# Kernel optimization log

Hardware: AMD Instinct MI355X
Metric: run time of the kernel (lower is better)

## Reference

```python
import jax, jax.numpy as jnp
import numpy as np

N_NODES = 4096
N_EDGES = 32768
IN_FEAT = 256
OUT_FEAT = 128
HID = 64
IN_HEAD = 64
OUT_HEAD = 5
NEG_SLOPE = 0.2
EPS = 1e-16


def setup_inputs() -> dict:
    key = jax.random.key(0)
    ks = jax.random.split(key, 12)
    x = jax.random.normal(ks[0], (N_NODES, IN_FEAT), dtype=jnp.float32)
    src = jax.random.randint(ks[1], (N_EDGES,), 0, N_NODES)
    dst = jax.random.randint(ks[2], (N_EDGES,), 0, N_NODES)
    edge_index = jnp.stack([src, dst]).astype(jnp.int64)
    s1 = 1.0 / np.sqrt(IN_FEAT)
    s2 = 1.0 / np.sqrt(HID * IN_HEAD)
    W1 = jax.random.normal(ks[3], (IN_FEAT, IN_HEAD * HID), dtype=jnp.float32) * s1
    att_src1 = jax.random.normal(ks[4], (IN_HEAD, HID), dtype=jnp.float32) * 0.1
    att_dst1 = jax.random.normal(ks[5], (IN_HEAD, HID), dtype=jnp.float32) * 0.1
    b1 = jnp.zeros((IN_HEAD * HID,), dtype=jnp.float32)
    W2 = jax.random.normal(ks[6], (IN_HEAD * HID, OUT_HEAD * OUT_FEAT), dtype=jnp.float32) * s2
    att_src2 = jax.random.normal(ks[7], (OUT_HEAD, OUT_FEAT), dtype=jnp.float32) * 0.1
    att_dst2 = jax.random.normal(ks[8], (OUT_HEAD, OUT_FEAT), dtype=jnp.float32) * 0.1
    b2 = jnp.zeros((OUT_FEAT,), dtype=jnp.float32)
    return {"x": x, "edge_index": edge_index, "W1": W1, "att_src1": att_src1,
            "att_dst1": att_dst1, "b1": b1, "W2": W2, "att_src2": att_src2,
            "att_dst2": att_dst2, "b2": b2}


def _gat_conv(x, W, att_src, att_dst, bias, src, dst, heads, out_c, concat):
    # x: [N, F_in]; returns [N, heads*out_c] (concat) or [N, out_c] (mean)
    n = x.shape[0]
    h = (x @ W).reshape(n, heads, out_c)                       # [N,H,C]
    a_src = jnp.sum(h * att_src, axis=-1)                      # [N,H]
    a_dst = jnp.sum(h * att_dst, axis=-1)                      # [N,H]
    e = jax.nn.leaky_relu(a_src[src] + a_dst[dst], NEG_SLOPE)  # [E,H]
    # segment softmax over edges grouped by destination node (PyG softmax)
    m = jax.ops.segment_max(e, dst, num_segments=n)            # [N,H]
    ex = jnp.exp(e - m[dst])
    denom = jax.ops.segment_sum(ex, dst, num_segments=n)       # [N,H]
    alpha = ex / (denom[dst] + EPS)                            # [E,H]
    out = jax.ops.segment_sum(alpha[:, :, None] * h[src], dst, num_segments=n)  # [N,H,C]
    out = out.reshape(n, heads * out_c) if concat else out.mean(axis=1)
    return out + bias


def reference(x, edge_index, W1, att_src1, att_dst1, b1, W2, att_src2, att_dst2, b2):
    n = x.shape[0]
    # PyG GATConv default: add self loops
    loop = jnp.arange(n, dtype=edge_index.dtype)
    src = jnp.concatenate([edge_index[0], loop])
    dst = jnp.concatenate([edge_index[1], loop])
    # dropout layers are identity in eval mode
    h = _gat_conv(x, W1, att_src1, att_dst1, b1, src, dst, IN_HEAD, HID, True)
    h = jax.nn.elu(h)
    h = _gat_conv(h, W2, att_src2, att_dst2, b2, src, dst, OUT_HEAD, OUT_FEAT, False)
    s = jnp.mean(h, axis=0)
    return jnp.tanh(s)
```

## Files before the change

### kernel.cpp

```cpp
#include <hip/hip_runtime.h>
#include <hip/hip_bf16.h>

#define N_NODES 4096
#define NE      32768
#define E_TOT   (NE + N_NODES)
#define IN_FEAT 256
#define HID     64
#define IN_HEAD 64
#define F1      4096
#define OUT_HEAD 5
#define OUT_FEAT 128
#define F2      640
#define NEG_SLOPE 0.2f
#define EPS_A   1e-16f

typedef __bf16 bf16;
typedef bf16 bf16x8 __attribute__((ext_vector_type(8)));
typedef bf16 bf16x4 __attribute__((ext_vector_type(4)));
typedef float f32x4 __attribute__((ext_vector_type(4)));

__device__ inline void async_cp16(bf16* lds, const bf16* g) {
    __builtin_amdgcn_global_load_lds(
        (const __attribute__((address_space(1))) unsigned int*)g,
        (__attribute__((address_space(3))) unsigned int*)lds, 16, 0, 0);
}

__global__ void hist_kernel(const int* __restrict__ edst, int* counts) {
    int e = blockIdx.x * 256 + threadIdx.x;
    if (e >= E_TOT) return;
    int d = (e < NE) ? edst[e] : (e - NE);
    atomicAdd(&counts[d], 1);
}

__global__ void scan_kernel(const int* __restrict__ counts,
                            int* __restrict__ row_start, int* __restrict__ cursor) {
    __shared__ int part[256];
    __shared__ int pre[257];
    int t = threadIdx.x;
    int base = t * 16;
    int local[16];
    int s = 0;
#pragma unroll
    for (int i = 0; i < 16; ++i) { local[i] = s; s += counts[base + i]; }
    part[t] = s;
    __syncthreads();
    if (t == 0) {
        int r = 0;
        for (int i = 0; i < 256; ++i) { pre[i] = r; r += part[i]; }
        pre[256] = r;
    }
    __syncthreads();
    int off = pre[t];
#pragma unroll
    for (int i = 0; i < 16; ++i) {
        int v = off + local[i];
        row_start[base + i] = v;
        cursor[base + i] = v;
    }
    if (t == 0) row_start[N_NODES] = pre[256];
}

__global__ void scatter_kernel(const int* __restrict__ esrc,
                               const int* __restrict__ edst,
                               int* cursor, int* __restrict__ srclist) {
    int e = blockIdx.x * 256 + threadIdx.x;
    if (e >= E_TOT) return;
    int d = (e < NE) ? edst[e] : (e - NE);
    int s = (e < NE) ? esrc[e] : (e - NE);
    int slot = atomicAdd(&cursor[d], 1);
    srclist[slot] = s;
}

#define PB_X   512
#define PB_W1  1024
#define PB_W2  2560
__global__ __launch_bounds__(256)
void prep_kernel(const float* __restrict__ x, bf16* __restrict__ xb,
                 const float* __restrict__ W1, bf16* __restrict__ W1T,
                 const float* __restrict__ W2, bf16* __restrict__ W2T,
                 const float* __restrict__ as1, const float* __restrict__ ad1,
                 bf16* __restrict__ w1s, bf16* __restrict__ w1d) {
    __shared__ float tile[32][33];
    int b = blockIdx.x, t = threadIdx.x;
    if (b < PB_X) {
        int i = b * 256 + t;
        f32x4 a = *(const f32x4*)(x + (size_t)i * 8);
        f32x4 c = *(const f32x4*)(x + (size_t)i * 8 + 4);
        bf16x8 r;
        r[0] = (bf16)a[0]; r[1] = (bf16)a[1]; r[2] = (bf16)a[2]; r[3] = (bf16)a[3];
        r[4] = (bf16)c[0]; r[5] = (bf16)c[1]; r[6] = (bf16)c[2]; r[7] = (bf16)c[3];
        *(bf16x8*)(xb + (size_t)i * 8) = r;
    } else if (b < PB_X + PB_W1 + PB_W2) {
        const float* S; bf16* D; int R, C, gx, gy;
        if (b < PB_X + PB_W1) {
            int bb = b - PB_X;
            S = W1; D = W1T; R = IN_FEAT; C = F1;
            gx = bb % (F1 / 32); gy = bb / (F1 / 32);
        } else {
            int bb = b - PB_X - PB_W1;
            S = W2; D = W2T; R = F1; C = F2;
            gx = bb % (F2 / 32); gy = bb / (F2 / 32);
        }
        int tx = t & 31, ty = t >> 5;
        int c0 = gx * 32, r0 = gy * 32;
#pragma unroll
        for (int i = 0; i < 4; ++i)
            tile[ty + i * 8][tx] = S[(size_t)(r0 + ty + i * 8) * C + c0 + tx];
        __syncthreads();
#pragma unroll
        for (int i = 0; i < 4; ++i)
            D[(size_t)(c0 + ty + i * 8) * R + r0 + tx] = (bf16)tile[tx][ty + i * 8];
    } else {
        int id = (b - PB_X - PB_W1 - PB_W2) * 256 + t;
        int k = id >> 6, h = id & 63;
        const float* wrow = W1 + (size_t)k * F1 + h * HID;
        const float* a1 = as1 + h * HID;
        const float* a2 = ad1 + h * HID;
        float s = 0.f, d = 0.f;
#pragma unroll 8
        for (int c = 0; c < HID; ++c) {
            float w = wrow[c];
            s += w * a1[c];
            d += w * a2[c];
        }
        w1s[id] = (bf16)s;
        w1d[id] = (bf16)d;
    }
}

template <int SPLITK, bool SWZ, typename TC>
__global__ __launch_bounds__(256)
void gemm128_kernel(const bf16* __restrict__ A, const bf16* __restrict__ BT,
                    TC* __restrict__ C, int M, int N, int K) {
    __shared__ bf16 As[128][64];
    __shared__ bf16 Bs[128][64];
    const int tid  = threadIdx.x;
    const int wave = tid >> 6, lane = tid & 63;
    const int quad = lane >> 4, lr = lane & 15;
    int nb, mb, zb;
    if constexpr (SWZ) {
        int bid = blockIdx.x;
        int xx = bid & 7, q = bid >> 3;
        int gp = q / 5; nb = q - gp * 5;
        int g = gp * 8 + xx;
        mb = g >> 2; zb = g & 3;
    } else {
        nb = blockIdx.x; mb = blockIdx.y; zb = blockIdx.z;
    }
    const int m0 = mb * 128, n0 = nb * 128;
    const int kchunk = K / SPLITK;
    const int kbeg = zb * kchunk;
    const int wm = (wave >> 1) * 64;
    const int wn = (wave & 1) * 64;
    TC* Cz = C + (size_t)zb * M * N;

    const int srow = lane >> 3;
    const int scol = ((lane & 7) ^ srow) * 8;
    const int xk = lr & 7;

    f32x4 acc[4][4] = {};

    for (int kk = 0; kk < kchunk; kk += 64) {
        int k0 = kbeg + kk;
#pragma unroll
        for (int c = 0; c < 4; ++c) {
            int r = wave * 32 + c * 8;
            async_cp16(&As[r][0], A + (size_t)(m0 + r + srow) * K + k0 + scol);
            async_cp16(&Bs[r][0], BT + (size_t)(n0 + r + srow) * K + k0 + scol);
        }
        __syncthreads();

#pragma unroll
        for (int ks = 0; ks < 2; ++ks) {
            int ch = ((ks * 4 + quad) ^ xk) * 8;
            bf16x8 af[4], bfr[4];
#pragma unroll
            for (int mt = 0; mt < 4; ++mt)
                af[mt] = *(const bf16x8*)(&As[wm + mt * 16 + lr][ch]);
#pragma unroll
            for (int nt = 0; nt < 4; ++nt)
                bfr[nt] = *(const bf16x8*)(&Bs[wn + nt * 16 + lr][ch]);
#pragma unroll
            for (int mt = 0; mt < 4; ++mt)
#pragma unroll
                for (int nt = 0; nt < 4; ++nt)
                    acc[mt][nt] = __builtin_amdgcn_mfma_f32_16x16x32_bf16(
                        af[mt], bfr[nt], acc[mt][nt], 0, 0, 0);
        }
        __syncthreads();
    }

#pragma unroll
    for (int mt = 0; mt < 4; ++mt)
#pragma unroll
        for (int nt = 0; nt < 4; ++nt) {
            int row0 = m0 + wm + mt * 16 + quad * 4;
            int col = n0 + wn + nt * 16 + lr;
#pragma unroll
            for (int r = 0; r < 4; ++r)
                Cz[(size_t)(row0 + r) * N + col] = (TC)acc[mt][nt][r];
        }
}

__global__ __launch_bounds__(256)
void gemv1_kernel(const float* __restrict__ x,
                  const bf16* __restrict__ w1s, const bf16* __restrict__ w1d,
                  float* __restrict__ a_src, float* __restrict__ a_dst) {
    int wave = threadIdx.x >> 6, lane = threadIdx.x & 63;
    int n = blockIdx.x * 4 + wave;
    const float* xr = x + (size_t)n * IN_FEAT;
    float s = 0.f, d = 0.f;
    for (int k0 = 0; k0 < IN_FEAT; k0 += 4) {
        f32x4 xv = *(const f32x4*)(xr + k0);
#pragma unroll
        for (int j = 0; j < 4; ++j) {
            float xs = xv[j];
            s += xs * (float)w1s[(k0 + j) * IN_HEAD + lane];
            d += xs * (float)w1d[(k0 + j) * IN_HEAD + lane];
        }
    }
    a_src[n * IN_HEAD + lane] = s;
    a_dst[n * IN_HEAD + lane] = d;
}

__global__ __launch_bounds__(64)
void agg1_kernel(const int* __restrict__ row_start,
                 const int* __restrict__ srclist,
                 const float* __restrict__ a_src, const float* __restrict__ a_dst,
                 const bf16* __restrict__ H1, const float* __restrict__ b1,
                 bf16* __restrict__ h_elu) {
    int bid = blockIdx.x;
    int c = bid & 7;
    int d = bid >> 3;
    int lane = threadIdx.x;
    int gh = c * 8 + (lane >> 3);
    int beg = row_start[d], deg = row_start[d + 1] - beg;
    float adst = a_dst[d * IN_HEAD + gh];
    int fbase = c * 512 + lane * 8;
    const float* asg = a_src + gh;

    auto SL = [&](int i) { return srclist[beg + (i < deg ? i : deg - 1)]; };

    int s0 = SL(0), s1 = SL(1), s2 = SL(2), s3 = SL(3);
    float la0 = asg[(size_t)s0 * IN_HEAD];
    bf16x8 v0 = *(const bf16x8*)(H1 + (size_t)s0 * F1 + fbase);
    float la1 = asg[(size_t)s1 * IN_HEAD];
    bf16x8 v1 = *(const bf16x8*)(H1 + (size_t)s1 * F1 + fbase);
    float la2 = asg[(size_t)s2 * IN_HEAD];
    bf16x8 v2 = *(const bf16x8*)(H1 + (size_t)s2 * F1 + fbase);
    float la3 = asg[(size_t)s3 * IN_HEAD];
    bf16x8 v3 = *(const bf16x8*)(H1 + (size_t)s3 * F1 + fbase);
    int s4 = SL(4), s5 = SL(5);

    float m = -1e30f, den = 0.f;
    float acc[8] = {};
    for (int i = 0; i < deg; ++i) {
        int sn = SL(i + 6);
        float la4 = asg[(size_t)s4 * IN_HEAD];
        bf16x8 v4 = *(const bf16x8*)(H1 + (size_t)s4 * F1 + fbase);

        float l = la0 + adst;
        l = l > 0.f ? l : NEG_SLOPE * l;
        if (l > m + 12.f) {
            float r = __expf(m - l);
            den *= r;
#pragma unroll
            for (int k = 0; k < 8; ++k) acc[k] *= r;
            m = l;
        }
        float w = __expf(l - m);
        den += w;
#pragma unroll
        for (int k = 0; k < 8; ++k) acc[k] += w * (float)v0[k];

        la0 = la1; v0 = v1;
        la1 = la2; v1 = v2;
        la2 = la3; v2 = v3;
        la3 = la4; v3 = v4;
        s4 = s5; s5 = sn;
    }
    float dinv = 1.f / (den + EPS_A);

    bf16x8 o;
#pragma unroll
    for (int j = 0; j < 8; ++j) {
        float v = acc[j] * dinv + b1[fbase + j];
        o[j] = (bf16)(v > 0.f ? v : (__expf(v) - 1.f));
    }
    *(bf16x8*)(h_elu + (size_t)d * F1 + fbase) = o;
}

__global__ __launch_bounds__(192)
void fold2_kernel(const bf16* __restrict__ Hp,
                  const float* __restrict__ as2, const float* __restrict__ ad2,
                  float* __restrict__ H2,
                  float* __restrict__ a_src, float* __restrict__ a_dst) {
    int n = blockIdx.x, t = threadIdx.x;
    if (t >= 160) return;
    int h = t >> 5;
    f32x4 sum = {};
#pragma unroll
    for (int z = 0; z < 4; ++z) {
        bf16x4 v = *(const bf16x4*)(Hp + (size_t)z * N_NODES * F2 + (size_t)n * F2 + t * 4);
        sum[0] += (float)v[0]; sum[1] += (float)v[1];
        sum[2] += (float)v[2]; sum[3] += (float)v[3];
    }
    *(f32x4*)(H2 + (size_t)n * F2 + t * 4) = sum;
    f32x4 ws = *(const f32x4*)(as2 + t * 4);
    f32x4 wd = *(const f32x4*)(ad2 + t * 4);
    float s = sum[0] * ws[0] + sum[1] * ws[1] + sum[2] * ws[2] + sum[3] * ws[3];
    float d = sum[0] * wd[0] + sum[1] * wd[1] + sum[2] * wd[2] + sum[3] * wd[3];
#pragma unroll
    for (int o = 1; o <= 16; o <<= 1) {
        s += __shfl_xor(s, o);
        d += __shfl_xor(d, o);
    }
    if ((t & 31) == 0) {
        a_src[n * OUT_HEAD + h] = s;
        a_dst[n * OUT_HEAD + h] = d;
    }
}

__global__ void stats2_kernel(const int* __restrict__ row_start,
                              const int* __restrict__ srclist,
                              const float* __restrict__ a_src,
                              const float* __restrict__ a_dst,
                              float* __restrict__ m2, float* __restrict__ dinv2) {
    int id = blockIdx.x * 256 + threadIdx.x;
    if (id >= N_NODES * OUT_HEAD) return;
    int d = id / OUT_HEAD, h = id - d * OUT_HEAD;
    int beg = row_start[d], deg = row_start[d + 1] - beg;
    float adst = a_dst[id];
    float m = -1e30f, den = 0.f;
    for (int i = 0; i < deg; ++i) {
        int s = srclist[beg + i];
        float l = a_src[s * OUT_HEAD + h] + adst;
        l = l > 0.f ? l : NEG_SLOPE * l;
        if (l > m) { den = den * __expf(m - l) + 1.f; m = l; }
        else den += __expf(l - m);
    }
    m2[id] = m;
    dinv2[id] = 1.f / (den + EPS_A);
}

__global__ void beta_kernel(const int* __restrict__ es, const int* __restrict__ ed,
                            const float* __restrict__ a_src, const float* __restrict__ a_dst,
                            const float* __restrict__ m2, const float* __restrict__ dinv2,
                            float* __restrict__ beta) {
    int id = blockIdx.x * 256 + threadIdx.x;
    if (id >= E_TOT * OUT_HEAD) return;
    int e = id / OUT_HEAD, h = id - e * OUT_HEAD;
    int s = (e < NE) ? es[e] : (e - NE);
    int d = (e < NE) ? ed[e] : (e - NE);
    float l = a_src[s * OUT_HEAD + h] + a_dst[d * OUT_HEAD + h];
    l = l > 0.f ? l : NEG_SLOPE * l;
    float alpha = __expf(l - m2[d * OUT_HEAD + h]) * dinv2[d * OUT_HEAD + h];
    atomicAdd(&beta[s * OUT_HEAD + h], alpha);
}

__global__ __launch_bounds__(256)
void wsum_kernel(const float* __restrict__ H2, const float* __restrict__ beta,
                 float* __restrict__ acc_out, const float* __restrict__ b2,
                 float* __restrict__ out, int* __restrict__ ticket) {
    __shared__ float buf[F2];
    __shared__ int lastblk;
    int t = threadIdx.x;
    int n0 = blockIdx.x * 32;
    int h = t >> 5;
    float a0 = 0.f, a1 = 0.f, a2 = 0.f, a3 = 0.f;
    if (t < 160) {
        for (int i = 0; i < 32; ++i) {
            int s = n0 + i;
            float bh = beta[s * OUT_HEAD + h];
            f32x4 v = *(const f32x4*)(H2 + (size_t)s * F2 + t * 4);
            a0 += bh * v[0]; a1 += bh * v[1];
            a2 += bh * v[2]; a3 += bh * v[3];
        }
        buf[t * 4 + 0] = a0; buf[t * 4 + 1] = a1;
        buf[t * 4 + 2] = a2; buf[t * 4 + 3] = a3;
    }
    __syncthreads();
    if (t < OUT_FEAT) {
        float s = 0.f;
#pragma unroll
        for (int hh = 0; hh < OUT_HEAD; ++hh) s += buf[hh * OUT_FEAT + t];
        atomicAdd(&acc_out[(blockIdx.x & 7) * OUT_FEAT + t], s);
    }
    __syncthreads();
    if (t == 0) {
        __threadfence();
        lastblk = (atomicAdd(ticket, 1) == (int)gridDim.x - 1);
    }
    __syncthreads();
    if (lastblk && t < OUT_FEAT) {
        float tot = 0.f;
#pragma unroll
        for (int k = 0; k < 8; ++k)
            tot += atomicAdd(&acc_out[k * OUT_FEAT + t], 0.0f);
        out[t] = tanhf(tot * (1.f / (OUT_HEAD * (float)N_NODES)) + b2[t]);
    }
}

extern "C" void kernel_launch(void* const* d_in, const int* in_sizes, int n_in,
                              void* d_out, int out_size, void* d_ws, size_t ws_size,
                              hipStream_t stream) {
    const float* x        = (const float*)d_in[0];
    const int*   ei       = (const int*)d_in[1];
    const float* W1       = (const float*)d_in[2];
    const float* att_src1 = (const float*)d_in[3];
    const float* att_dst1 = (const float*)d_in[4];
    const float* b1       = (const float*)d_in[5];
    const float* W2       = (const float*)d_in[6];
    const float* att_src2 = (const float*)d_in[7];
    const float* att_dst2 = (const float*)d_in[8];
    const float* b2       = (const float*)d_in[9];
    float* out = (float*)d_out;

    const int* esrc = ei;
    const int* edst = ei + NE;

    char* p = (char*)d_ws;
    auto bump = [&](size_t bytes) {
        void* r = (void*)p;
        p += (bytes + 255) & ~(size_t)255;
        return r;
    };
    bf16*  H1     = (bf16*)bump((size_t)N_NODES * F1 * 2);
    bf16*  h_elu  = (bf16*)bump((size_t)N_NODES * F1 * 2);
    float* H2     = (float*)bump((size_t)N_NODES * F2 * 4);
    bf16*  xb     = (bf16*)bump((size_t)N_NODES * IN_FEAT * 2);
    bf16*  W1T    = (bf16*)bump((size_t)F1 * IN_FEAT * 2);
    bf16*  W2T    = (bf16*)bump((size_t)F2 * F1 * 2);
    bf16*  w1s    = (bf16*)bump((size_t)IN_FEAT * IN_HEAD * 2);
    bf16*  w1d    = (bf16*)bump((size_t)IN_FEAT * IN_HEAD * 2);
    float* a_src1 = (float*)bump((size_t)N_NODES * IN_HEAD * 4);
    float* a_dst1 = (float*)bump((size_t)N_NODES * IN_HEAD * 4);
    float* a_src2 = (float*)bump((size_t)N_NODES * OUT_HEAD * 4);
    float* a_dst2 = (float*)bump((size_t)N_NODES * OUT_HEAD * 4);
    float* m2     = (float*)bump((size_t)N_NODES * OUT_HEAD * 4);
    float* dinv2  = (float*)bump((size_t)N_NODES * OUT_HEAD * 4);
    int*   row_start = (int*)bump((N_NODES + 1) * 4);
    int*   cursor  = (int*)bump(N_NODES * 4);
    int*   srclist = (int*)bump(E_TOT * 4);
    size_t zbytes = N_NODES * 4 + N_NODES * OUT_HEAD * 4 + 8 * OUT_FEAT * 4 + 4;
    int*   counts = (int*)bump(zbytes);
    float* beta    = (float*)((char*)counts + N_NODES * 4);
    float* acc_out = beta + N_NODES * OUT_HEAD;
    int*   ticket  = (int*)(acc_out + 8 * OUT_FEAT);
    bf16* Hp = H1;

    hipMemsetAsync(counts, 0, zbytes, stream);

    hist_kernel<<<(E_TOT + 255) / 256, 256, 0, stream>>>(edst, counts);
    scan_kernel<<<1, 256, 0, stream>>>(counts, row_start, cursor);
    scatter_kernel<<<(E_TOT + 255) / 256, 256, 0, stream>>>(
        esrc, edst, cursor, srclist);

    prep_kernel<<<PB_X + PB_W1 + PB_W2 + 64, 256, 0, stream>>>(
        x, xb, W1, W1T, W2, W2T, att_src1, att_dst1, w1s, w1d);

    gemm128_kernel<1, false, bf16>
        <<<dim3(F1 / 128, N_NODES / 128, 1), 256, 0, stream>>>(
        xb, W1T, H1, N_NODES, F1, IN_FEAT);
    gemv1_kernel<<<N_NODES / 4, 256, 0, stream>>>(x, w1s, w1d, a_src1, a_dst1);
    agg1_kernel<<<N_NODES * 8, 64, 0, stream>>>(
        row_start, srclist, a_src1, a_dst1, H1, b1, h_elu);

    gemm128_kernel<4, true, bf16><<<640, 256, 0, stream>>>(
        h_elu, W2T, Hp, N_NODES, F2, F1);
    fold2_kernel<<<N_NODES, 192, 0, stream>>>(
        Hp, att_src2, att_dst2, H2, a_src2, a_dst2);
    stats2_kernel<<<(N_NODES * OUT_HEAD + 255) / 256, 256, 0, stream>>>(
        row_start, srclist, a_src2, a_dst2, m2, dinv2);
    beta_kernel<<<(E_TOT * OUT_HEAD + 255) / 256, 256, 0, stream>>>(
        esrc, edst, a_src2, a_dst2, m2, dinv2, beta);
    wsum_kernel<<<N_NODES / 32, 256, 0, stream>>>(
        H2, beta, acc_out, b2, out, ticket);
}
```

Measured before the change: 238.6 us.

## Fuse CSR build into one block, raise split-K to 8, drop memset

Replaces the histogram, scan and scatter kernels plus the memset with a single 1024-thread block that counts in LDS, scans with wave shuffles and scatters. The second GEMM goes from split-K 4 to split-K 8 with 1280 blocks writing into a separate partial buffer, and fold2 sums eight partials. Zeroing of beta, acc_out and ticket moves into stats2 and beta_kernel, and stats2 prefetches source indices and uses a lazy-rescale online softmax. The aim is fewer launches and more GEMM parallelism, at the cost of a serial single-block CSR build and extra partial-sum traffic.

```diff
diff --git a/kernel.cpp b/kernel.cpp
--- a/kernel.cpp
+++ b/kernel.cpp
@@ -25,50 +25,53 @@
         (__attribute__((address_space(3))) unsigned int*)lds, 16, 0, 0);
 }
 
-__global__ void hist_kernel(const int* __restrict__ edst, int* counts) {
-    int e = blockIdx.x * 256 + threadIdx.x;
-    if (e >= E_TOT) return;
-    int d = (e < NE) ? edst[e] : (e - NE);
-    atomicAdd(&counts[d], 1);
-}
-
-__global__ void scan_kernel(const int* __restrict__ counts,
-                            int* __restrict__ row_start, int* __restrict__ cursor) {
-    __shared__ int part[256];
-    __shared__ int pre[257];
+__global__ __launch_bounds__(1024)
+void csr_kernel(const int* __restrict__ esrc, const int* __restrict__ edst,
+                int* __restrict__ row_start, int* __restrict__ srclist) {
+    __shared__ int cnt[N_NODES];
+    __shared__ int woff[17];
     int t = threadIdx.x;
-    int base = t * 16;
-    int local[16];
-    int s = 0;
-#pragma unroll
-    for (int i = 0; i < 16; ++i) { local[i] = s; s += counts[base + i]; }
-    part[t] = s;
+    int lane = t & 63, wid = t >> 6;
+    for (int i = t; i < N_NODES; i += 1024) cnt[i] = 0;
+    __syncthreads();
+    for (int e = t; e < E_TOT; e += 1024) {
+        int d = (e < NE) ? edst[e] : (e - NE);
+        atomicAdd(&cnt[d], 1);
+    }
+    __syncthreads();
+    int b0 = t * 4;
+    int c0 = cnt[b0], c1 = cnt[b0 + 1], c2 = cnt[b0 + 2], c3 = cnt[b0 + 3];
+    int s = c0 + c1 + c2 + c3;
+    int v = s;
+#pragma unroll
+    for (int o = 1; o < 64; o <<= 1) {
+        int u = __shfl_up(v, o);
+        if (lane >= o) v += u;
+    }
+    if (lane == 63) woff[wid + 1] = v;
     __syncthreads();
     if (t == 0) {
-        int r = 0;
-        for (int i = 0; i < 256; ++i) { pre[i] = r; r += part[i]; }
-        pre[256] = r;
-    }
-    __syncthreads();
-    int off = pre[t];
-#pragma unroll
-    for (int i = 0; i < 16; ++i) {
-        int v = off + local[i];
-        row_start[base + i] = v;
-        cursor[base + i] = v;
-    }
-    if (t == 0) row_start[N_NODES] = pre[256];
-}
-
-__global__ void scatter_kernel(const int* __restrict__ esrc,
-                               const int* __restrict__ edst,
-                               int* cursor, int* __restrict__ srclist) {
-    int e = blockIdx.x * 256 + threadIdx.x;
-    if (e >= E_TOT) return;
-    int d = (e < NE) ? edst[e] : (e - NE);
-    int s = (e < NE) ? esrc[e] : (e - NE);
-    int slot = atomicAdd(&cursor[d], 1);
-    srclist[slot] = s;
+        woff[0] = 0;
+        for (int w = 1; w <= 16; ++w) woff[w] += woff[w - 1];
+        row_start[N_NODES] = woff[16];
+    }
+    __syncthreads();
+    int excl = woff[wid] + v - s;
+    row_start[b0]     = excl;
+    row_start[b0 + 1] = excl + c0;
+    row_start[b0 + 2] = excl + c0 + c1;
+    row_start[b0 + 3] = excl + c0 + c1 + c2;
+    cnt[b0]     = excl;
+    cnt[b0 + 1] = excl + c0;
+    cnt[b0 + 2] = excl + c0 + c1;
+    cnt[b0 + 3] = excl + c0 + c1 + c2;
+    __syncthreads();
+    for (int e = t; e < E_TOT; e += 1024) {
+        int d  = (e < NE) ? edst[e] : (e - NE);
+        int sv = (e < NE) ? esrc[e] : (e - NE);
+        int slot = atomicAdd(&cnt[d], 1);
+        srclist[slot] = sv;
+    }
 }
 
 #define PB_X   512
@@ -140,10 +143,18 @@
     int nb, mb, zb;
     if constexpr (SWZ) {
         int bid = blockIdx.x;
-        int xx = bid & 7, q = bid >> 3;
-        int gp = q / 5; nb = q - gp * 5;
-        int g = gp * 8 + xx;
-        mb = g >> 2; zb = g & 3;
+        if constexpr (SPLITK == 8) {
+            zb = bid & 7;
+            int q = bid >> 3;
+            int gp = q / 5;
+            nb = q - gp * 5;
+            mb = gp;
+        } else {
+            int xx = bid & 7, q = bid >> 3;
+            int gp = q / 5; nb = q - gp * 5;
+            int g = gp * 8 + xx;
+            mb = g >> 2; zb = g & 3;
+        }
     } else {
         nb = blockIdx.x; mb = blockIdx.y; zb = blockIdx.z;
     }
@@ -300,7 +311,7 @@
     int h = t >> 5;
     f32x4 sum = {};
 #pragma unroll
-    for (int z = 0; z < 4; ++z) {
+    for (int z = 0; z < 8; ++z) {
         bf16x4 v = *(const bf16x4*)(Hp + (size_t)z * N_NODES * F2 + (size_t)n * F2 + t * 4);
         sum[0] += (float)v[0]; sum[1] += (float)v[1];
         sum[2] += (float)v[2]; sum[3] += (float)v[3];
@@ -325,19 +336,26 @@
                               const int* __restrict__ srclist,
                               const float* __restrict__ a_src,
                               const float* __restrict__ a_dst,
-                              float* __restrict__ m2, float* __restrict__ dinv2) {
+                              float* __restrict__ m2, float* __restrict__ dinv2,
+                              float* __restrict__ beta) {
     int id = blockIdx.x * 256 + threadIdx.x;
     if (id >= N_NODES * OUT_HEAD) return;
+    beta[id] = 0.f;
     int d = id / OUT_HEAD, h = id - d * OUT_HEAD;
     int beg = row_start[d], deg = row_start[d + 1] - beg;
     float adst = a_dst[id];
+    auto SL = [&](int i) { return srclist[beg + (i < deg ? i : deg - 1)]; };
+    int s0 = SL(0), s1 = SL(1);
+    float la0 = a_src[s0 * OUT_HEAD + h];
     float m = -1e30f, den = 0.f;
     for (int i = 0; i < deg; ++i) {
-        int s = srclist[beg + i];
-        float l = a_src[s * OUT_HEAD + h] + adst;
+        int s2 = SL(i + 2);
+        float la1 = a_src[s1 * OUT_HEAD + h];
+        float l = la0 + adst;
         l = l > 0.f ? l : NEG_SLOPE * l;
-        if (l > m) { den = den * __expf(m - l) + 1.f; m = l; }
-        else den += __expf(l - m);
+        if (l > m + 12.f) { den *= __expf(m - l); m = l; }
+        den += __expf(l - m);
+        la0 = la1; s1 = s2;
     }
     m2[id] = m;
     dinv2[id] = 1.f / (den + EPS_A);
@@ -346,8 +364,11 @@
 __global__ void beta_kernel(const int* __restrict__ es, const int* __restrict__ ed,
                             const float* __restrict__ a_src, const float* __restrict__ a_dst,
                             const float* __restrict__ m2, const float* __restrict__ dinv2,
-                            float* __restrict__ beta) {
+                            float* __restrict__ beta,
+                            float* __restrict__ acc_out, int* __restrict__ ticket) {
     int id = blockIdx.x * 256 + threadIdx.x;
+    if (id < 8 * OUT_FEAT) acc_out[id] = 0.f;
+    else if (id == 8 * OUT_FEAT) *ticket = 0;
     if (id >= E_TOT * OUT_HEAD) return;
     int e = id / OUT_HEAD, h = id - e * OUT_HEAD;
     int s = (e < NE) ? es[e] : (e - NE);
@@ -427,6 +448,7 @@
     };
     bf16*  H1     = (bf16*)bump((size_t)N_NODES * F1 * 2);
     bf16*  h_elu  = (bf16*)bump((size_t)N_NODES * F1 * 2);
+    bf16*  Hp     = (bf16*)bump((size_t)8 * N_NODES * F2 * 2);
     float* H2     = (float*)bump((size_t)N_NODES * F2 * 4);
     bf16*  xb     = (bf16*)bump((size_t)N_NODES * IN_FEAT * 2);
     bf16*  W1T    = (bf16*)bump((size_t)F1 * IN_FEAT * 2);
@@ -440,21 +462,12 @@
     float* m2     = (float*)bump((size_t)N_NODES * OUT_HEAD * 4);
     float* dinv2  = (float*)bump((size_t)N_NODES * OUT_HEAD * 4);
     int*   row_start = (int*)bump((N_NODES + 1) * 4);
-    int*   cursor  = (int*)bump(N_NODES * 4);
     int*   srclist = (int*)bump(E_TOT * 4);
-    size_t zbytes = N_NODES * 4 + N_NODES * OUT_HEAD * 4 + 8 * OUT_FEAT * 4 + 4;
-    int*   counts = (int*)bump(zbytes);
-    float* beta    = (float*)((char*)counts + N_NODES * 4);
-    float* acc_out = beta + N_NODES * OUT_HEAD;
-    int*   ticket  = (int*)(acc_out + 8 * OUT_FEAT);
-    bf16* Hp = H1;
-
-    hipMemsetAsync(counts, 0, zbytes, stream);
-
-    hist_kernel<<<(E_TOT + 255) / 256, 256, 0, stream>>>(edst, counts);
-    scan_kernel<<<1, 256, 0, stream>>>(counts, row_start, cursor);
-    scatter_kernel<<<(E_TOT + 255) / 256, 256, 0, stream>>>(
-        esrc, edst, cursor, srclist);
+    float* beta    = (float*)bump((size_t)N_NODES * OUT_HEAD * 4);
+    float* acc_out = (float*)bump((size_t)8 * OUT_FEAT * 4);
+    int*   ticket  = (int*)bump(4);
+
+    csr_kernel<<<1, 1024, 0, stream>>>(esrc, edst, row_start, srclist);
 
     prep_kernel<<<PB_X + PB_W1 + PB_W2 + 64, 256, 0, stream>>>(
         x, xb, W1, W1T, W2, W2T, att_src1, att_dst1, w1s, w1d);
@@ -466,14 +479,14 @@
     agg1_kernel<<<N_NODES * 8, 64, 0, stream>>>(
         row_start, srclist, a_src1, a_dst1, H1, b1, h_elu);
 
-    gemm128_kernel<4, true, bf16><<<640, 256, 0, stream>>>(
+    gemm128_kernel<8, true, bf16><<<1280, 256, 0, stream>>>(
         h_elu, W2T, Hp, N_NODES, F2, F1);
     fold2_kernel<<<N_NODES, 192, 0, stream>>>(
         Hp, att_src2, att_dst2, H2, a_src2, a_dst2);
     stats2_kernel<<<(N_NODES * OUT_HEAD + 255) / 256, 256, 0, stream>>>(
-        row_start, srclist, a_src2, a_dst2, m2, dinv2);
+        row_start, srclist, a_src2, a_dst2, m2, dinv2, beta);
     beta_kernel<<<(E_TOT * OUT_HEAD + 255) / 256, 256, 0, stream>>>(
-        esrc, edst, a_src2, a_dst2, m2, dinv2, beta);
+        esrc, edst, a_src2, a_dst2, m2, dinv2, beta, acc_out, ticket);
     wsum_kernel<<<N_NODES / 32, 256, 0, stream>>>(
         H2, beta, acc_out, b2, out, ticket);
 }
```

Measured after the change: 273.3 us. +14.6%, slower.

## Raise layer-2 GEMM split-K to 8, fold memset into kernels, pipeline softmax stats

Applied to the files above, without the earlier changes.

The second-layer GEMM now splits K eight ways over 1280 blocks instead of four ways over 640. Its partials go to a dedicated buffer, and fold2 sums eight partial slices. The memset that zeroed beta, acc_out and ticket is replaced by zeroing inside stats2 and beta_kernel, leaving only the counts memset. stats2 software-pipelines its srclist/a_src loads and rescales the running max lazily, only when a logit exceeds it by a threshold. The intent is more GEMM parallelism on the many CUs and less launch and latency overhead, in exchange for twice the partial-sum traffic.

```diff
diff --git a/kernel.cpp b/kernel.cpp
--- a/kernel.cpp
+++ b/kernel.cpp
@@ -140,10 +140,11 @@
     int nb, mb, zb;
     if constexpr (SWZ) {
         int bid = blockIdx.x;
-        int xx = bid & 7, q = bid >> 3;
-        int gp = q / 5; nb = q - gp * 5;
-        int g = gp * 8 + xx;
-        mb = g >> 2; zb = g & 3;
+        zb = bid & 7;
+        int q = bid >> 3;
+        int gp = q / 5;
+        nb = q - gp * 5;
+        mb = gp;
     } else {
         nb = blockIdx.x; mb = blockIdx.y; zb = blockIdx.z;
     }
@@ -300,7 +301,7 @@
     int h = t >> 5;
     f32x4 sum = {};
 #pragma unroll
-    for (int z = 0; z < 4; ++z) {
+    for (int z = 0; z < 8; ++z) {
         bf16x4 v = *(const bf16x4*)(Hp + (size_t)z * N_NODES * F2 + (size_t)n * F2 + t * 4);
         sum[0] += (float)v[0]; sum[1] += (float)v[1];
         sum[2] += (float)v[2]; sum[3] += (float)v[3];
@@ -325,19 +326,26 @@
                               const int* __restrict__ srclist,
                               const float* __restrict__ a_src,
                               const float* __restrict__ a_dst,
-                              float* __restrict__ m2, float* __restrict__ dinv2) {
+                              float* __restrict__ m2, float* __restrict__ dinv2,
+                              float* __restrict__ beta) {
     int id = blockIdx.x * 256 + threadIdx.x;
     if (id >= N_NODES * OUT_HEAD) return;
+    beta[id] = 0.f;
     int d = id / OUT_HEAD, h = id - d * OUT_HEAD;
     int beg = row_start[d], deg = row_start[d + 1] - beg;
     float adst = a_dst[id];
+    auto SL = [&](int i) { return srclist[beg + (i < deg ? i : deg - 1)]; };
+    int s0 = SL(0), s1 = SL(1);
+    float la0 = a_src[s0 * OUT_HEAD + h];
     float m = -1e30f, den = 0.f;
     for (int i = 0; i < deg; ++i) {
-        int s = srclist[beg + i];
-        float l = a_src[s * OUT_HEAD + h] + adst;
+        int s2 = SL(i + 2);
+        float la1 = a_src[s1 * OUT_HEAD + h];
+        float l = la0 + adst;
         l = l > 0.f ? l : NEG_SLOPE * l;
-        if (l > m) { den = den * __expf(m - l) + 1.f; m = l; }
-        else den += __expf(l - m);
+        if (l > m + 12.f) { den *= __expf(m - l); m = l; }
+        den += __expf(l - m);
+        la0 = la1; s1 = s2;
     }
     m2[id] = m;
     dinv2[id] = 1.f / (den + EPS_A);
@@ -346,8 +354,11 @@
 __global__ void beta_kernel(const int* __restrict__ es, const int* __restrict__ ed,
                             const float* __restrict__ a_src, const float* __restrict__ a_dst,
                             const float* __restrict__ m2, const float* __restrict__ dinv2,
-                            float* __restrict__ beta) {
+                            float* __restrict__ beta,
+                            float* __restrict__ acc_out, int* __restrict__ ticket) {
     int id = blockIdx.x * 256 + threadIdx.x;
+    if (id < 8 * OUT_FEAT) acc_out[id] = 0.f;
+    else if (id == 8 * OUT_FEAT) *ticket = 0;
     if (id >= E_TOT * OUT_HEAD) return;
     int e = id / OUT_HEAD, h = id - e * OUT_HEAD;
     int s = (e < NE) ? es[e] : (e - NE);
@@ -427,6 +438,7 @@
     };
     bf16*  H1     = (bf16*)bump((size_t)N_NODES * F1 * 2);
     bf16*  h_elu  = (bf16*)bump((size_t)N_NODES * F1 * 2);
+    bf16*  Hp     = (bf16*)bump((size_t)8 * N_NODES * F2 * 2);
     float* H2     = (float*)bump((size_t)N_NODES * F2 * 4);
     bf16*  xb     = (bf16*)bump((size_t)N_NODES * IN_FEAT * 2);
     bf16*  W1T    = (bf16*)bump((size_t)F1 * IN_FEAT * 2);
@@ -442,15 +454,12 @@
     int*   row_start = (int*)bump((N_NODES + 1) * 4);
     int*   cursor  = (int*)bump(N_NODES * 4);
     int*   srclist = (int*)bump(E_TOT * 4);
-    size_t zbytes = N_NODES * 4 + N_NODES * OUT_HEAD * 4 + 8 * OUT_FEAT * 4 + 4;
-    int*   counts = (int*)bump(zbytes);
-    float* beta    = (float*)((char*)counts + N_NODES * 4);
-    float* acc_out = beta + N_NODES * OUT_HEAD;
-    int*   ticket  = (int*)(acc_out + 8 * OUT_FEAT);
-    bf16* Hp = H1;
-
-    hipMemsetAsync(counts, 0, zbytes, stream);
-
+    int*   counts  = (int*)bump(N_NODES * 4);
+    float* beta    = (float*)bump((size_t)N_NODES * OUT_HEAD * 4);
+    float* acc_out = (float*)bump((size_t)8 * OUT_FEAT * 4);
+    int*   ticket  = (int*)bump(4);
+
+    hipMemsetAsync(counts, 0, N_NODES * 4, stream);
     hist_kernel<<<(E_TOT + 255) / 256, 256, 0, stream>>>(edst, counts);
     scan_kernel<<<1, 256, 0, stream>>>(counts, row_start, cursor);
     scatter_kernel<<<(E_TOT + 255) / 256, 256, 0, stream>>>(
@@ -466,14 +475,14 @@
     agg1_kernel<<<N_NODES * 8, 64, 0, stream>>>(
         row_start, srclist, a_src1, a_dst1, H1, b1, h_elu);
 
-    gemm128_kernel<4, true, bf16><<<640, 256, 0, stream>>>(
+    gemm128_kernel<8, true, bf16><<<1280, 256, 0, stream>>>(
         h_elu, W2T, Hp, N_NODES, F2, F1);
     fold2_kernel<<<N_NODES, 192, 0, stream>>>(
         Hp, att_src2, att_dst2, H2, a_src2, a_dst2);
     stats2_kernel<<<(N_NODES * OUT_HEAD + 255) / 256, 256, 0, stream>>>(
-        row_start, srclist, a_src2, a_dst2, m2, dinv2);
+        row_start, srclist, a_src2, a_dst2, m2, dinv2, beta);
     beta_kernel<<<(E_TOT * OUT_HEAD + 255) / 256, 256, 0, stream>>>(
-        esrc, edst, a_src2, a_dst2, m2, dinv2, beta);
+        esrc, edst, a_src2, a_dst2, m2, dinv2, beta, acc_out, ticket);
     wsum_kernel<<<N_NODES / 32, 256, 0, stream>>>(
         H2, beta, acc_out, b2, out, ticket);
 }
```

Result: slower. 244.5 us (+2.5%).
